# Optimization experiments

Hardware: AMD Instinct MI355X
Metric: run time of the kernel (lower is better)

## Reference

```python
import jax, jax.numpy as jnp
import numpy as np

N_NODES = 1000
ALPHA = 0.1  # LeakyReLU negative slope


def gcn_conv(x, edge_index, W, b):
    """PyG GCNConv: add self-loops, symmetric deg^{-1/2} normalization,
    linear transform, scatter-add aggregation at destination, plus bias."""
    n = x.shape[0]
    src, dst = edge_index[0], edge_index[1]
    loop = jnp.arange(n, dtype=src.dtype)
    src = jnp.concatenate([src, loop])
    dst = jnp.concatenate([dst, loop])
    deg = jax.ops.segment_sum(jnp.ones(src.shape[0], dtype=x.dtype), dst, num_segments=n)
    dinv = jnp.where(deg > 0, jax.lax.rsqrt(jnp.maximum(deg, 1e-12)), 0.0)
    norm = dinv[src] * dinv[dst]                     # [E+n]
    h = x @ W                                        # [n, out]
    out = jax.ops.segment_sum(norm[:, None] * h[src], dst, num_segments=n)
    return out + b


def leaky_relu(x):
    return jnp.where(x > 0, x, ALPHA * x)


def setup_inputs() -> dict:
    key = jax.random.key(0)
    ks = jax.random.split(key, 16)
    F_in, D, H = 128, 512, 256
    x = jax.random.normal(ks[0], (N_NODES, F_in), dtype=jnp.float32)
    edge_index = jax.random.randint(ks[1], (2, 64000), 0, N_NODES, dtype=jnp.int64)

    def lin(k, fan_in, fan_out):
        s = 1.0 / np.sqrt(fan_in)
        kw, kb = jax.random.split(k)
        W = jax.random.uniform(kw, (fan_in, fan_out), minval=-s, maxval=s, dtype=jnp.float32)
        b = jax.random.uniform(kb, (fan_out,), minval=-s, maxval=s, dtype=jnp.float32)
        return W, b

    W1, b1 = lin(ks[2], F_in, D)
    W2, b2 = lin(ks[3], D, D)
    W3, b3 = lin(ks[4], D, D)
    Wd1, bd1 = lin(ks[5], N_NODES * D, H)
    Wd2, bd2 = lin(ks[6], H, H)
    Wd3, bd3 = lin(ks[7], H, H)
    Wd4, bd4 = lin(ks[8], H, 1)
    return {"x": x, "edge_index": edge_index,
            "W1": W1, "b1": b1, "W2": W2, "b2": b2, "W3": W3, "b3": b3,
            "Wd1": Wd1, "bd1": bd1, "Wd2": Wd2, "bd2": bd2,
            "Wd3": Wd3, "bd3": bd3, "Wd4": Wd4, "bd4": bd4}


def reference(x, edge_index, W1, b1, W2, b2, W3, b3,
              Wd1, bd1, Wd2, bd2, Wd3, bd3, Wd4, bd4):
    h = jnp.tanh(gcn_conv(x, edge_index, W1, b1))
    h = jnp.tanh(gcn_conv(h, edge_index, W2, b2))
    h = jnp.tanh(gcn_conv(h, edge_index, W3, b3))
    f = h.reshape(-1)                                # flatten [N*D]
    f = leaky_relu(f @ Wd1 + bd1)
    f = leaky_relu(f @ Wd2 + bd2)
    f = leaky_relu(f @ Wd3 + bd3)
    out = f @ Wd4 + bd4                              # [1]
    return out
```

## Files before the change

kernel.cpp:

```cpp
#include <hip/hip_runtime.h>
#include <math.h>

#define N_NODES 1000
#define E_EDGES 64000
#define STRIDE  256

typedef float fx4 __attribute__((ext_vector_type(4)));

__device__ inline float lrelu(float v){ return v > 0.f ? v : 0.1f * v; }

__global__ __launch_bounds__(1024)
void kA(const int* __restrict__ src, const int* __restrict__ dst,
        const float* __restrict__ x, int* __restrict__ cnt,
        int* __restrict__ csr, int* __restrict__ built,
        const float* __restrict__ W1, const float* __restrict__ b1,
        const float* __restrict__ W2, float* __restrict__ hs2){
  __shared__ float dinv_lds[1024];
  __shared__ fx4 gsum[4][8][32];
  __shared__ float xa[4 * 128];
  __shared__ float h1s[4 * 512];
  __shared__ fx4 red[7][4][128];
  int b = blockIdx.x, t = threadIdx.x;
  if (b < 125){
    if (t < 512){
      int e = b * 512 + t;
      int s = src[e], d = dst[e];
      int pos = atomicAdd(&cnt[d], 1);
      if (pos < STRIDE) csr[(d << 8) + pos] = s;
    }
    __syncthreads();
    if (t == 0)
      __hip_atomic_fetch_add(built, 1, __ATOMIC_RELEASE, __HIP_MEMORY_SCOPE_AGENT);
  }
  if (t == 0){
    while (__hip_atomic_load(built, __ATOMIC_ACQUIRE, __HIP_MEMORY_SCOPE_AGENT) < 125)
      __builtin_amdgcn_s_sleep(16);
  }
  __syncthreads();
  dinv_lds[t] = (t < N_NODES) ? rsqrtf((float)(cnt[t] + 1)) : 0.f;
  __syncthreads();
  {
    int q = t >> 8, tt = t & 255;
    int c = tt & 31, sl = tt >> 5;
    int n = b * 4 + q;
    int m = cnt[n]; if (m > STRIDE) m = STRIDE;
    const fx4* x4 = (const fx4*)x;
    const int* row = csr + (n << 8);
    fx4 acc = {0.f, 0.f, 0.f, 0.f};
    if (sl == 0) acc = dinv_lds[n] * x4[n * 32 + c];
    for (int i = sl; i < m; i += 8){
      int sv = row[i];
      acc += dinv_lds[sv] * x4[sv * 32 + c];
    }
    gsum[q][sl][c] = acc;
    __syncthreads();
    if (sl < 4) gsum[q][sl][c] += gsum[q][sl + 4][c];
    __syncthreads();
    if (sl < 2) gsum[q][sl][c] += gsum[q][sl + 2][c];
    __syncthreads();
    if (sl == 0)
      ((fx4*)xa)[q * 32 + c] = dinv_lds[n] * (gsum[q][0][c] + gsum[q][1][c]);
    __syncthreads();
  }
  int cq = t & 127, kh = t >> 7;
  {
    fx4 a0 = {0,0,0,0}, a1 = {0,0,0,0}, a2 = {0,0,0,0}, a3 = {0,0,0,0};
    int kb = kh * 16;
    const fx4* Wp = (const fx4*)W1 + (size_t)kb * 128 + cq;
    #pragma unroll
    for (int k = 0; k < 16; ++k){
      fx4 w = Wp[k * 128];
      float h0 = xa[0 * 128 + kb + k], h1 = xa[1 * 128 + kb + k];
      float h2 = xa[2 * 128 + kb + k], h3 = xa[3 * 128 + kb + k];
      a0 += h0 * w; a1 += h1 * w; a2 += h2 * w; a3 += h3 * w;
    }
    if (kh > 0){
      red[kh-1][0][cq] = a0; red[kh-1][1][cq] = a1;
      red[kh-1][2][cq] = a2; red[kh-1][3][cq] = a3;
    }
    __syncthreads();
    if (kh == 0){
      #pragma unroll
      for (int s = 0; s < 7; ++s){
        a0 += red[s][0][cq]; a1 += red[s][1][cq];
        a2 += red[s][2][cq]; a3 += red[s][3][cq];
      }
      fx4 bb = ((const fx4*)b1)[cq];
      fx4* H = (fx4*)h1s;
      fx4 o;
      o.x=tanhf(a0.x+bb.x); o.y=tanhf(a0.y+bb.y); o.z=tanhf(a0.z+bb.z); o.w=tanhf(a0.w+bb.w); H[0*128+cq]=o;
      o.x=tanhf(a1.x+bb.x); o.y=tanhf(a1.y+bb.y); o.z=tanhf(a1.z+bb.z); o.w=tanhf(a1.w+bb.w); H[1*128+cq]=o;
      o.x=tanhf(a2.x+bb.x); o.y=tanhf(a2.y+bb.y); o.z=tanhf(a2.z+bb.z); o.w=tanhf(a2.w+bb.w); H[2*128+cq]=o;
      o.x=tanhf(a3.x+bb.x); o.y=tanhf(a3.y+bb.y); o.z=tanhf(a3.z+bb.z); o.w=tanhf(a3.w+bb.w); H[3*128+cq]=o;
    }
    __syncthreads();
  }
  {
    fx4 a0 = {0,0,0,0}, a1 = {0,0,0,0}, a2 = {0,0,0,0}, a3 = {0,0,0,0};
    int kb = kh * 64;
    const fx4* Wp = (const fx4*)W2 + (size_t)kb * 128 + cq;
    #pragma unroll 8
    for (int k = 0; k < 64; ++k){
      fx4 w = Wp[k * 128];
      float h0 = h1s[0 * 512 + kb + k], h1 = h1s[1 * 512 + kb + k];
      float h2 = h1s[2 * 512 + kb + k], h3 = h1s[3 * 512 + kb + k];
      a0 += h0 * w; a1 += h1 * w; a2 += h2 * w; a3 += h3 * w;
    }
    if (kh > 0){
      red[kh-1][0][cq] = a0; red[kh-1][1][cq] = a1;
      red[kh-1][2][cq] = a2; red[kh-1][3][cq] = a3;
    }
    __syncthreads();
    if (kh == 0){
      #pragma unroll
      for (int s = 0; s < 7; ++s){
        a0 += red[s][0][cq]; a1 += red[s][1][cq];
        a2 += red[s][2][cq]; a3 += red[s][3][cq];
      }
      int r0 = b * 4;
      fx4* O = (fx4*)hs2;
      O[(size_t)(r0 + 0) * 128 + cq] = a0 * dinv_lds[r0 + 0];
      O[(size_t)(r0 + 1) * 128 + cq] = a1 * dinv_lds[r0 + 1];
      O[(size_t)(r0 + 2) * 128 + cq] = a2 * dinv_lds[r0 + 2];
      O[(size_t)(r0 + 3) * 128 + cq] = a3 * dinv_lds[r0 + 3];
    }
  }
}

__global__ __launch_bounds__(1024)
void kB(const float* __restrict__ hs_in, const int* __restrict__ cnt,
        const int* __restrict__ csr, const float* __restrict__ bias,
        const float* __restrict__ W, float* __restrict__ hs_out){
  __shared__ float h2l[4 * 512];
  __shared__ fx4 hpart[4][128];
  __shared__ fx4 red[7][4][128];
  int b = blockIdx.x, t = threadIdx.x;
  {
    int q = t >> 8, tt = t & 255;
    int c = tt & 127, half = tt >> 7;
    int n = b * 4 + q;
    int m = cnt[n]; if (m > STRIDE) m = STRIDE;
    const fx4* h4 = (const fx4*)hs_in;
    const int* row = csr + (n << 8);
    fx4 s = {0.f, 0.f, 0.f, 0.f};
    if (half == 0) s = h4[n * 128 + c];
    int i = half;
    for (; i + 6 < m; i += 8){
      int s0 = row[i], s1 = row[i + 2], s2 = row[i + 4], s3 = row[i + 6];
      s += h4[s0 * 128 + c] + h4[s1 * 128 + c]
         + h4[s2 * 128 + c] + h4[s3 * 128 + c];
    }
    for (; i < m; i += 2) s += h4[row[i] * 128 + c];
    if (half == 1) hpart[q][c] = s;
    __syncthreads();
    if (half == 0){
      s += hpart[q][c];
      float dn = rsqrtf((float)(m + 1));
      fx4 bb = ((const fx4*)bias)[c];
      fx4 o;
      o.x = tanhf(dn * s.x + bb.x);
      o.y = tanhf(dn * s.y + bb.y);
      o.z = tanhf(dn * s.z + bb.z);
      o.w = tanhf(dn * s.w + bb.w);
      ((fx4*)h2l)[q * 128 + c] = o;
    }
    __syncthreads();
  }
  int cq = t & 127, kh = t >> 7;
  fx4 a0 = {0,0,0,0}, a1 = {0,0,0,0}, a2 = {0,0,0,0}, a3 = {0,0,0,0};
  int kb = kh * 64;
  const fx4* Wp = (const fx4*)W + (size_t)kb * 128 + cq;
  #pragma unroll 8
  for (int k = 0; k < 64; ++k){
    fx4 w = Wp[k * 128];
    float h0 = h2l[0 * 512 + kb + k], h1 = h2l[1 * 512 + kb + k];
    float h2 = h2l[2 * 512 + kb + k], h3 = h2l[3 * 512 + kb + k];
    a0 += h0 * w; a1 += h1 * w; a2 += h2 * w; a3 += h3 * w;
  }
  if (kh > 0){
    red[kh-1][0][cq] = a0; red[kh-1][1][cq] = a1;
    red[kh-1][2][cq] = a2; red[kh-1][3][cq] = a3;
  }
  __syncthreads();
  if (kh == 0){
    #pragma unroll
    for (int s = 0; s < 7; ++s){
      a0 += red[s][0][cq]; a1 += red[s][1][cq];
      a2 += red[s][2][cq]; a3 += red[s][3][cq];
    }
    int r0 = b * 4;
    fx4* O = (fx4*)hs_out;
    O[(size_t)(r0 + 0) * 128 + cq] = a0 * rsqrtf((float)(cnt[r0 + 0] + 1));
    O[(size_t)(r0 + 1) * 128 + cq] = a1 * rsqrtf((float)(cnt[r0 + 1] + 1));
    O[(size_t)(r0 + 2) * 128 + cq] = a2 * rsqrtf((float)(cnt[r0 + 2] + 1));
    O[(size_t)(r0 + 3) * 128 + cq] = a3 * rsqrtf((float)(cnt[r0 + 3] + 1));
  }
}

__global__ __launch_bounds__(1024)
void kC(const float* __restrict__ hs_in, const int* __restrict__ cnt,
        const int* __restrict__ csr, const float* __restrict__ bias,
        const float* __restrict__ Wd1, float* __restrict__ partial,
        int* __restrict__ done,
        const float* __restrict__ bd1,
        const float* __restrict__ Wd2, const float* __restrict__ bd2,
        const float* __restrict__ Wd3, const float* __restrict__ bd3,
        const float* __restrict__ Wd4, const float* __restrict__ bd4,
        float* __restrict__ out){
  __shared__ float f_lds[2048];
  __shared__ fx4 red4[1024];
  __shared__ float y[256];
  __shared__ int flag;
  int b = blockIdx.x, t = threadIdx.x;
  if (b < 8){
    const fx4* w2 = (const fx4*)Wd2;
    const fx4* w3 = (const fx4*)Wd3;
    fx4 v0 = w2[b * 2048 + t] + w3[b * 2048 + t];
    fx4 v1 = w2[b * 2048 + 1024 + t] + w3[b * 2048 + 1024 + t];
    float dm = v0.x + v1.x;
    asm volatile("" :: "v"(dm));
  }
  {
    int q = t >> 8, tt = t & 255;
    int cc = tt & 127, half = tt >> 7;
    int n = b * 4 + q;
    int m = cnt[n]; if (m > STRIDE) m = STRIDE;
    const fx4* h4 = (const fx4*)hs_in;
    const int* row = csr + (n << 8);
    fx4 s = {0.f, 0.f, 0.f, 0.f};
    if (half == 0) s = h4[n * 128 + cc];
    int i = half;
    for (; i + 6 < m; i += 8){
      int s0 = row[i], s1 = row[i + 2], s2 = row[i + 4], s3 = row[i + 6];
      s += h4[s0 * 128 + cc] + h4[s1 * 128 + cc]
         + h4[s2 * 128 + cc] + h4[s3 * 128 + cc];
    }
    for (; i < m; i += 2) s += h4[row[i] * 128 + cc];
    if (half == 1) ((fx4*)red4)[q * 128 + cc] = s;
    __syncthreads();
    if (half == 0){
      s += ((fx4*)red4)[q * 128 + cc];
      float dn = rsqrtf((float)(m + 1));
      fx4 bb = ((const fx4*)bias)[cc];
      fx4 o;
      o.x = tanhf(dn * s.x + bb.x);
      o.y = tanhf(dn * s.y + bb.y);
      o.z = tanhf(dn * s.z + bb.z);
      o.w = tanhf(dn * s.w + bb.w);
      ((fx4*)f_lds)[q * 128 + cc] = o;
    }
    __syncthreads();
  }
  int r = t >> 6, c = t & 63;
  const fx4* W4 = (const fx4*)Wd1 + (size_t)b * 131072 + c;
  fx4 acc = {0.f, 0.f, 0.f, 0.f};
  #pragma unroll 8
  for (int it = 0; it < 128; ++it){
    int i2 = it * 16 + r;
    acc += f_lds[i2] * __builtin_nontemporal_load(&W4[(size_t)i2 * 64]);
  }
  red4[t] = acc;
  __syncthreads();
  if (t < 512) red4[t] += red4[t + 512];
  __syncthreads();
  if (t < 256) red4[t] += red4[t + 256];
  __syncthreads();
  if (t < 128) red4[t] += red4[t + 128];
  __syncthreads();
  if (t < 64) ((fx4*)(partial + b * 256))[t] = red4[t] + red4[t + 64];
  __syncthreads();
  if (t == 0){
    __threadfence();
    int old = atomicAdd(done, 1);
    flag = (old == 249);
  }
  __syncthreads();
  if (!flag) return;
  __threadfence();
  float* sm = (float*)red4;
  int c2 = t & 255, h = t >> 8;
  float sum = 0.f;
  for (int bb2 = h; bb2 < 250; bb2 += 4) sum += partial[bb2 * 256 + c2];
  sm[t] = sum;
  __syncthreads();
  if (t < 512) sm[t] += sm[t + 512];
  __syncthreads();
  if (t < 256) y[t] = lrelu(sm[t] + sm[t + 256] + bd1[t]);
  __syncthreads();
  float a = 0.f;
  #pragma unroll 4
  for (int i3 = h * 64; i3 < h * 64 + 64; ++i3) a += y[i3] * Wd2[i3 * 256 + c2];
  sm[t] = a;
  __syncthreads();
  if (t < 512) sm[t] += sm[t + 512];
  __syncthreads();
  if (t < 256) y[t] = lrelu(sm[t] + sm[t + 256] + bd2[t]);
  __syncthreads();
  a = 0.f;
  #pragma unroll 4
  for (int i3 = h * 64; i3 < h * 64 + 64; ++i3) a += y[i3] * Wd3[i3 * 256 + c2];
  sm[t] = a;
  __syncthreads();
  if (t < 512) sm[t] += sm[t + 512];
  __syncthreads();
  if (t < 256) y[t] = lrelu(sm[t] + sm[t + 256] + bd3[t]);
  __syncthreads();
  sm[t] = (t < 256) ? y[t] * Wd4[t] : 0.f;
  __syncthreads();
  for (int off = 128; off > 0; off >>= 1){
    if (t < off) sm[t] += sm[t + off];
    __syncthreads();
  }
  if (t == 0) out[0] = sm[0] + bd4[0];
}


extern "C" void kernel_launch(void* const* d_in, const int* in_sizes, int n_in,
                              void* d_out, int out_size, void* d_ws, size_t ws_size,
                              hipStream_t stream) {
  const float* x   = (const float*)d_in[0];
  const int*   ei  = (const int*)  d_in[1];
  const float* W1  = (const float*)d_in[2];  const float* b1  = (const float*)d_in[3];
  const float* W2  = (const float*)d_in[4];  const float* b2  = (const float*)d_in[5];
  const float* W3  = (const float*)d_in[6];  const float* b3  = (const float*)d_in[7];
  const float* Wd1 = (const float*)d_in[8];  const float* bd1 = (const float*)d_in[9];
  const float* Wd2 = (const float*)d_in[10]; const float* bd2 = (const float*)d_in[11];
  const float* Wd3 = (const float*)d_in[12]; const float* bd3 = (const float*)d_in[13];
  const float* Wd4 = (const float*)d_in[14]; const float* bd4 = (const float*)d_in[15];
  float* out = (float*)d_out;

  const int* src = ei;
  const int* dst = ei + E_EDGES;

  char* ws = (char*)d_ws;
  int*   cnt     = (int*)  (ws + 0);
  int*   done    = (int*)  (ws + 4096);
  int*   built   = (int*)  (ws + 4160);
  int*   csr     = (int*)  (ws + 8192);
  float* hsA     = (float*)(ws + 1114112);
  float* hsB     = (float*)(ws + 1114112 + 2097152);
  float* partial = (float*)(ws + 1114112 + 2 * 2097152);

  (void)hipMemsetAsync(ws, 0, 8192, stream);
  kA<<<250, 1024, 0, stream>>>(src, dst, x, cnt, csr, built, W1, b1, W2, hsA);
  kB<<<250, 1024, 0, stream>>>(hsA, cnt, csr, b2, W3, hsB);
  kC<<<250, 1024, 0, stream>>>(hsB, cnt, csr, b3, Wd1, partial, done,
                               bd1, Wd2, bd2, Wd3, bd3, Wd4, bd4, out);
}
```

Measured before the change: 215.7 us.

## Build degree histogram and CSR redundantly per block, drop grid barrier and memset

Each of the 250 blocks now scans all 64000 edges itself, building a full degree histogram in LDS and collecting the source lists for its own four destination nodes. This removes the global-atomic CSR build, the spin-wait grid barrier across blocks, and the separate hipMemsetAsync launch. Block 0 resets the done counter and each block writes its own cnt/csr rows for the later kernels. The cost is redundant edge reads and LDS atomics in every block, and the reset of done assumes kA finishes before kC uses it.

```diff
diff --git a/kernel.cpp b/kernel.cpp
--- a/kernel.cpp
+++ b/kernel.cpp
@@ -12,44 +12,60 @@
 __global__ __launch_bounds__(1024)
 void kA(const int* __restrict__ src, const int* __restrict__ dst,
         const float* __restrict__ x, int* __restrict__ cnt,
-        int* __restrict__ csr, int* __restrict__ built,
+        int* __restrict__ csr, int* __restrict__ done,
         const float* __restrict__ W1, const float* __restrict__ b1,
         const float* __restrict__ W2, float* __restrict__ hs2){
+  __shared__ int   hist[1024];
+  __shared__ int   own_cnt[4];
+  __shared__ int   own_src[4][STRIDE];
   __shared__ float dinv_lds[1024];
-  __shared__ fx4 gsum[4][8][32];
+  __shared__ fx4   gsum[4][8][32];
   __shared__ float xa[4 * 128];
   __shared__ float h1s[4 * 512];
-  __shared__ fx4 red[7][4][128];
+  __shared__ fx4   red[7][4][128];
   int b = blockIdx.x, t = threadIdx.x;
-  if (b < 125){
-    if (t < 512){
-      int e = b * 512 + t;
-      int s = src[e], d = dst[e];
-      int pos = atomicAdd(&cnt[d], 1);
-      if (pos < STRIDE) csr[(d << 8) + pos] = s;
-    }
-    __syncthreads();
-    if (t == 0)
-      __hip_atomic_fetch_add(built, 1, __ATOMIC_RELEASE, __HIP_MEMORY_SCOPE_AGENT);
-  }
-  if (t == 0){
-    while (__hip_atomic_load(built, __ATOMIC_ACQUIRE, __HIP_MEMORY_SCOPE_AGENT) < 125)
-      __builtin_amdgcn_s_sleep(16);
-  }
-  __syncthreads();
-  dinv_lds[t] = (t < N_NODES) ? rsqrtf((float)(cnt[t] + 1)) : 0.f;
-  __syncthreads();
+
+  hist[t] = 0;
+  if (t < 4) own_cnt[t] = 0;
+  if (t == 0 && b == 0) *done = 0;
+  __syncthreads();
+  {
+    const int4* s4p = (const int4*)src;
+    const int4* d4p = (const int4*)dst;
+    for (int i = t; i < E_EDGES / 4; i += 1024){
+      int4 d4 = d4p[i];
+      int4 s4 = s4p[i];
+      #pragma unroll
+      for (int j = 0; j < 4; ++j){
+        int d = (j == 0) ? d4.x : (j == 1) ? d4.y : (j == 2) ? d4.z : d4.w;
+        int s = (j == 0) ? s4.x : (j == 1) ? s4.y : (j == 2) ? s4.z : s4.w;
+        atomicAdd(&hist[d], 1);
+        if ((d >> 2) == b){
+          int pos = atomicAdd(&own_cnt[d & 3], 1);
+          if (pos < STRIDE) own_src[d & 3][pos] = s;
+        }
+      }
+    }
+  }
+  __syncthreads();
+  dinv_lds[t] = (t < N_NODES) ? rsqrtf((float)(hist[t] + 1)) : 0.f;
+  if (t < 4) cnt[b * 4 + t] = own_cnt[t];
+  for (int i = t; i < 4 * STRIDE; i += 1024){
+    int q = i >> 8, pos = i & 255;
+    if (pos < own_cnt[q]) csr[((b * 4 + q) << 8) + pos] = own_src[q][pos];
+  }
+  __syncthreads();
+
   {
     int q = t >> 8, tt = t & 255;
     int c = tt & 31, sl = tt >> 5;
     int n = b * 4 + q;
-    int m = cnt[n]; if (m > STRIDE) m = STRIDE;
+    int m = own_cnt[q]; if (m > STRIDE) m = STRIDE;
     const fx4* x4 = (const fx4*)x;
-    const int* row = csr + (n << 8);
     fx4 acc = {0.f, 0.f, 0.f, 0.f};
     if (sl == 0) acc = dinv_lds[n] * x4[n * 32 + c];
     for (int i = sl; i < m; i += 8){
-      int sv = row[i];
+      int sv = own_src[q][i];
       acc += dinv_lds[sv] * x4[sv * 32 + c];
     }
     gsum[q][sl][c] = acc;
@@ -335,14 +351,12 @@
   char* ws = (char*)d_ws;
   int*   cnt     = (int*)  (ws + 0);
   int*   done    = (int*)  (ws + 4096);
-  int*   built   = (int*)  (ws + 4160);
   int*   csr     = (int*)  (ws + 8192);
   float* hsA     = (float*)(ws + 1114112);
   float* hsB     = (float*)(ws + 1114112 + 2097152);
   float* partial = (float*)(ws + 1114112 + 2 * 2097152);
 
-  (void)hipMemsetAsync(ws, 0, 8192, stream);
-  kA<<<250, 1024, 0, stream>>>(src, dst, x, cnt, csr, built, W1, b1, W2, hsA);
+  kA<<<250, 1024, 0, stream>>>(src, dst, x, cnt, csr, done, W1, b1, W2, hsA);
   kB<<<250, 1024, 0, stream>>>(hsA, cnt, csr, b2, W3, hsB);
   kC<<<250, 1024, 0, stream>>>(hsB, cnt, csr, b3, Wd1, partial, done,
                                bd1, Wd2, bd2, Wd3, bd3, Wd4, bd4, out);
```

Measured after the change: 181.1 us, median of 2. 1.19x faster.
